# Kernel tuning notes

Measured on AMD Instinct MI355X. Metric: run time of the kernel, lower is better.

The kernel has to match this reference:

```python
import jax, jax.numpy as jnp
import numpy as np

HEAD_SIZE = 64


def setup_inputs() -> dict:
    key = jax.random.key(0)
    ks = jax.random.split(key, 4)
    B, S, H, D = 8, 4096, 768, HEAD_SIZE
    scale = 1.0 / np.sqrt(H)
    return {
        "x": jax.random.normal(ks[0], (B, S, H), dtype=jnp.float32),
        "Wq": jax.random.normal(ks[1], (H, D), dtype=jnp.float32) * scale,
        "bq": jnp.zeros((D,), dtype=jnp.float32),
        "Wk": jax.random.normal(ks[2], (H, D), dtype=jnp.float32) * scale,
        "bk": jnp.zeros((D,), dtype=jnp.float32),
        "Wv": jax.random.normal(ks[3], (H, D), dtype=jnp.float32) * scale,
        "bv": jnp.zeros((D,), dtype=jnp.float32),
    }


def reference(x, Wq, bq, Wk, bk, Wv, bv):
    # x: [B, S, H]
    B, S, H = x.shape
    D = Wq.shape[1]
    q = x @ Wq + bq  # [B, S, D]
    k = x @ Wk + bk
    v = x @ Wv + bv
    # naive full score matrix [B, S, S]
    scores = jnp.einsum("bsd,btd->bst", q, k)
    causal = jnp.tril(jnp.ones((S, S), dtype=bool))  # lower-triangular mask
    scores = jnp.where(causal[None, :, :], scores, -jnp.inf)
    attn = jax.nn.softmax(scores / jnp.sqrt(jnp.float32(D)), axis=-1)
    # dropout is identity in eval/deterministic reference
    out = jnp.einsum("bst,btd->bsd", attn, v)  # [B, S, D]
    return out
```

## Files before the change

kernel.cpp:

```cpp
#include <hip/hip_runtime.h>

typedef unsigned short u16;
typedef __bf16 bf16_t;
typedef bf16_t bf16x8 __attribute__((ext_vector_type(8)));
typedef float f32x4 __attribute__((ext_vector_type(4)));
typedef u16 u16x8 __attribute__((ext_vector_type(8)));

#define B_ 8
#define S_ 4096
#define H_ 768
#define M_ (B_ * S_)

__device__ __forceinline__ u16 f2b(float f) {
  unsigned u = __float_as_uint(f);
  u += 0x7fffu + ((u >> 16) & 1u);
  return (u16)(u >> 16);
}

__device__ __forceinline__ void gl_lds16(const void* g, void* l) {
  __builtin_amdgcn_global_load_lds(
      (const __attribute__((address_space(1))) void*)g,
      (__attribute__((address_space(3))) void*)l, 16, 0, 0);
}

__global__ __launch_bounds__(256) void wconv_k(const float* __restrict__ Wq,
                                               const float* __restrict__ Wk,
                                               const float* __restrict__ Wv,
                                               u16* __restrict__ WbT) {
  __shared__ float wt[64 * 68];
  const int tid = threadIdx.x;
  int mat = blockIdx.x / 12;
  int k0 = (blockIdx.x % 12) * 64;
  const float* W = (mat == 0) ? Wq : ((mat == 1) ? Wk : Wv);
  int r = tid >> 2, c0 = (tid & 3) * 16;
  const float* src = W + (size_t)(k0 + r) * 64 + c0;
#pragma unroll
  for (int j = 0; j < 16; j += 4)
    *(float4*)&wt[r * 68 + c0 + j] = *(const float4*)(src + j);
  __syncthreads();
  int d = tid >> 2;
  u16* dst = WbT + (size_t)(mat * 64 + d) * 768 + k0 + c0;
  u16x8 o0, o1;
#pragma unroll
  for (int j = 0; j < 8; ++j) o0[j] = f2b(wt[(c0 + j) * 68 + d]);
#pragma unroll
  for (int j = 0; j < 8; ++j) o1[j] = f2b(wt[(c0 + 8 + j) * 68 + d]);
  *(u16x8*)dst = o0;
  *(u16x8*)(dst + 8) = o1;
}

__global__ __launch_bounds__(256) void qkv_k(const float* __restrict__ x,
                                             const u16* __restrict__ WbT,
                                             const float* __restrict__ bq,
                                             const float* __restrict__ bk,
                                             const float* __restrict__ bv,
                                             u16* __restrict__ qb,
                                             u16* __restrict__ kb,
                                             u16* __restrict__ vbT) {
  __shared__ __align__(16) u16 smem[2 * 2560 + 2 * 7680];
  const int tid = threadIdx.x;
  const int w = tid >> 6, ln = tid & 15, qd = (tid >> 4) & 3;
  const int row0 = blockIdx.x * 64;

  const f32x4 z4 = {0.f, 0.f, 0.f, 0.f};
  f32x4 acc[4][3];
#pragma unroll
  for (int rt = 0; rt < 4; ++rt)
#pragma unroll
    for (int ct = 0; ct < 3; ++ct) acc[rt][ct] = z4;

  const int xr = tid >> 2, xc = (tid & 3) * 8;
  float4 xf0, xf1;
  u16x8 wf[3];

  auto load_t = [&](int kt) {
    const float* sx = x + (size_t)(row0 + xr) * 768 + kt * 32 + xc;
    xf0 = *(const float4*)sx;
    xf1 = *(const float4*)(sx + 4);
#pragma unroll
    for (int i = 0; i < 3; ++i) {
      int c = i * 256 + tid;
      int r = c >> 2, off = (c & 3) * 8;
      wf[i] = *(const u16x8*)(WbT + (size_t)r * 768 + kt * 32 + off);
    }
  };

  load_t(0);
  for (int kt = 0; kt < 24; ++kt) {
    u16* xs = smem + (kt & 1) * 2560;
    u16* wsb = smem + 5120 + (kt & 1) * 7680;
    {
      u16x8 v;
      v[0] = f2b(xf0.x); v[1] = f2b(xf0.y); v[2] = f2b(xf0.z); v[3] = f2b(xf0.w);
      v[4] = f2b(xf1.x); v[5] = f2b(xf1.y); v[6] = f2b(xf1.z); v[7] = f2b(xf1.w);
      *(u16x8*)&xs[xr * 40 + xc] = v;
#pragma unroll
      for (int i = 0; i < 3; ++i) {
        int c = i * 256 + tid;
        int r = c >> 2, off = (c & 3) * 8;
        *(u16x8*)&wsb[r * 40 + off] = wf[i];
      }
    }
    if (kt < 23) load_t(kt + 1);
    __syncthreads();
    bf16x8 af[4], bfr[3];
#pragma unroll
    for (int rt = 0; rt < 4; ++rt)
      af[rt] = *(const bf16x8*)&xs[(rt * 16 + ln) * 40 + qd * 8];
#pragma unroll
    for (int ct = 0; ct < 3; ++ct)
      bfr[ct] = *(const bf16x8*)&wsb[(w * 48 + ct * 16 + ln) * 40 + qd * 8];
#pragma unroll
    for (int rt = 0; rt < 4; ++rt)
#pragma unroll
      for (int ct = 0; ct < 3; ++ct)
        acc[rt][ct] = __builtin_amdgcn_mfma_f32_16x16x32_bf16(
            af[rt], bfr[ct], acc[rt][ct], 0, 0, 0);
    __syncthreads();
  }

  u16* vt = smem;
#pragma unroll
  for (int ct = 0; ct < 3; ++ct) {
    int col = w * 48 + ct * 16 + ln;
    int mat = col >> 6, d = col & 63;
    if (mat < 2) {
      const float* bp = (mat == 0) ? bq : bk;
      u16* op = (mat == 0) ? qb : kb;
      float bias = bp[d];
      float scale = (mat == 0) ? 0.18033688011112042f : 1.0f;
#pragma unroll
      for (int rt = 0; rt < 4; ++rt)
#pragma unroll
        for (int r = 0; r < 4; ++r)
          op[(size_t)(row0 + rt * 16 + qd * 4 + r) * 64 + d] =
              f2b((acc[rt][ct][r] + bias) * scale);
    } else {
      float bias = bv[d];
#pragma unroll
      for (int rt = 0; rt < 4; ++rt)
#pragma unroll
        for (int r = 0; r < 4; ++r)
          vt[d * 72 + rt * 16 + qd * 4 + r] = f2b(acc[rt][ct][r] + bias);
    }
  }
  __syncthreads();
  {
    int d = tid >> 2, so = (tid & 3) * 16;
    int b = row0 >> 12, s0 = row0 & 4095;
    u16* dst = vbT + ((size_t)b * 64 + d) * 4096 + s0 + so;
    *(u16x8*)dst = *(const u16x8*)&vt[d * 72 + so];
    *(u16x8*)(dst + 8) = *(const u16x8*)&vt[d * 72 + so + 8];
  }
}

__global__ __launch_bounds__(256) void attn_k(const u16* __restrict__ qb,
                                              const u16* __restrict__ kb,
                                              const u16* __restrict__ vbT,
                                              float* __restrict__ po0,
                                              float* __restrict__ po1,
                                              float* __restrict__ pl0,
                                              float* __restrict__ pl1) {
  __shared__ __align__(16) u16 ks[2][4096];
  __shared__ __align__(16) u16 vs[2][4096];
  __shared__ __align__(16) u16 ps[4 * 16 * 88];
  const int tid = threadIdx.x;
  const int w = tid >> 6, ln = tid & 15, qd = (tid >> 4) & 3;
  const int id = blockIdx.x;
  int b, qi, tstart, tcount;
  if (id < 256) {
    b = id & 7; qi = 32 + (id >> 3); tstart = 0; tcount = 32;
  } else if (id < 512) {
    b = id & 7; qi = 63 - ((id - 256) >> 3); tstart = 32; tcount = qi - 31;
  } else {
    b = id & 7; qi = 31 - ((id - 512) >> 3); tstart = 0; tcount = qi + 1;
  }
  const int q0 = qi * 64, q0w = q0 + w * 16;
  const int base = b * S_;
  const u16* kg = kb + (size_t)base * 64;
  const u16* vg = vbT + (size_t)b * 64 * 4096;

  bf16x8 qf[2];
  {
    const u16* qrow = qb + (size_t)(base + q0w + ln) * 64;
    qf[0] = *(const bf16x8*)(qrow + qd * 8);
    qf[1] = *(const bf16x8*)(qrow + 32 + qd * 8);
  }
  const f32x4 z4 = {0.f, 0.f, 0.f, 0.f};
  f32x4 o[4] = {z4, z4, z4, z4};
  float lp[4] = {0.f, 0.f, 0.f, 0.f};
  u16* psw = ps + w * (16 * 88);
  const int lr = (tid & 63) >> 3, csl = tid & 7;

  auto prefetch = [&](int bufi, int tile) {
    const u16* kt_ = kg + (size_t)tile * 4096;
    const u16* vt_ = vg + tile * 64;
#pragma unroll
    for (int i = 0; i < 2; ++i) {
      int r0 = w * 16 + i * 8;
      int r = r0 + lr;
      int c = csl ^ (r & 7);
      gl_lds16(kt_ + r * 64 + c * 8, &ks[bufi][r0 * 64]);
      gl_lds16(vt_ + (size_t)r * 4096 + c * 8, &vs[bufi][r0 * 64]);
    }
  };

  prefetch(0, tstart);
  int buf = 0;
  for (int it = 0; it < tcount; ++it) {
    __syncthreads();
    if (it + 1 < tcount) prefetch(buf ^ 1, tstart + it + 1);
    const int t0a = (tstart + it) * 64;

    f32x4 s[4] = {z4, z4, z4, z4};
#pragma unroll
    for (int kc = 0; kc < 2; ++kc) {
      int cs = (kc * 4 + qd) ^ (ln & 7);
#pragma unroll
      for (int nt = 0; nt < 4; ++nt) {
        bf16x8 bfr = *(const bf16x8*)&ks[buf][(nt * 16 + ln) * 64 + cs * 8];
        s[nt] = __builtin_amdgcn_mfma_f32_16x16x32_bf16(qf[kc], bfr, s[nt], 0, 0, 0);
      }
    }
    if (t0a == q0) {
#pragma unroll
      for (int nt = 0; nt < 4; ++nt) {
        int tg = t0a + nt * 16 + ln;
#pragma unroll
        for (int r = 0; r < 4; ++r)
          if (tg > q0w + qd * 4 + r) s[nt][r] = -INFINITY;
      }
    }
#pragma unroll
    for (int nt = 0; nt < 4; ++nt)
#pragma unroll
      for (int r = 0; r < 4; ++r) {
        float p = __builtin_amdgcn_exp2f(s[nt][r]);
        lp[r] += p;
        psw[(qd * 4 + r) * 88 + nt * 16 + ln] = f2b(p);
      }
#pragma unroll
    for (int kc = 0; kc < 2; ++kc) {
      bf16x8 afr = *(const bf16x8*)&psw[ln * 88 + kc * 32 + qd * 8];
      int cs = (kc * 4 + qd) ^ (ln & 7);
#pragma unroll
      for (int nt = 0; nt < 4; ++nt) {
        bf16x8 bfr = *(const bf16x8*)&vs[buf][(nt * 16 + ln) * 64 + cs * 8];
        o[nt] = __builtin_amdgcn_mfma_f32_16x16x32_bf16(afr, bfr, o[nt], 0, 0, 0);
      }
    }
    buf ^= 1;
  }

#pragma unroll
  for (int r = 0; r < 4; ++r) {
    float v = lp[r];
    v += __shfl_xor(v, 1); v += __shfl_xor(v, 2);
    v += __shfl_xor(v, 4); v += __shfl_xor(v, 8);
    lp[r] = v;
  }
  float* op = (tstart == 0) ? po0 : po1;
  float* lpt = (tstart == 0) ? pl0 : pl1;
#pragma unroll
  for (int r = 0; r < 4; ++r) {
    int row = base + q0w + qd * 4 + r;
#pragma unroll
    for (int nt = 0; nt < 4; ++nt)
      op[(size_t)row * 64 + nt * 16 + ln] = o[nt][r];
    if (ln == 0) lpt[row] = lp[r];
  }
}

__global__ __launch_bounds__(256) void comb_k(const float* __restrict__ po0,
                                              const float* __restrict__ po1,
                                              const float* __restrict__ pl0,
                                              const float* __restrict__ pl1,
                                              float* __restrict__ out) {
  int idx = blockIdx.x * 256 + threadIdx.x;
  int r = idx >> 4, d0 = (idx & 15) * 4;
  int qi = (r & 4095) >> 6;
  float4 a = *(const float4*)(po0 + (size_t)r * 64 + d0);
  float l = pl0[r];
  if (qi >= 32) {
    float4 c = *(const float4*)(po1 + (size_t)r * 64 + d0);
    a.x += c.x; a.y += c.y; a.z += c.z; a.w += c.w;
    l += pl1[r];
  }
  float inv = 1.0f / l;
  a.x *= inv; a.y *= inv; a.z *= inv; a.w *= inv;
  *(float4*)(out + (size_t)r * 64 + d0) = a;
}

extern "C" void kernel_launch(void* const* d_in, const int* in_sizes, int n_in,
                              void* d_out, int out_size, void* d_ws, size_t ws_size,
                              hipStream_t stream) {
  const float* x  = (const float*)d_in[0];
  const float* Wq = (const float*)d_in[1];
  const float* bq = (const float*)d_in[2];
  const float* Wk = (const float*)d_in[3];
  const float* bk = (const float*)d_in[4];
  const float* Wv = (const float*)d_in[5];
  const float* bv = (const float*)d_in[6];
  float* out = (float*)d_out;

  char* wsp = (char*)d_ws;
  u16* WbT = (u16*)wsp;
  u16* qb  = (u16*)(wsp + 294912);
  u16* kb  = (u16*)(wsp + 4489216);
  u16* vbT = (u16*)(wsp + 8683520);
  float* po0 = (float*)(wsp + 12877824);
  float* po1 = (float*)(wsp + 21266432);
  float* pl0 = (float*)(wsp + 29655040);
  float* pl1 = (float*)(wsp + 29786112);

  hipLaunchKernelGGL(wconv_k, dim3(36), dim3(256), 0, stream, Wq, Wk, Wv, WbT);
  hipLaunchKernelGGL(qkv_k, dim3(512), dim3(256), 0, stream,
                     x, WbT, bq, bk, bv, qb, kb, vbT);
  hipLaunchKernelGGL(attn_k, dim3(768), dim3(256), 0, stream,
                     qb, kb, vbT, po0, po1, pl0, pl1);
  hipLaunchKernelGGL(comb_k, dim3(2048), dim3(256), 0, stream,
                     po0, po1, pl0, pl1, out);
}
```

Measured before the change: 226.3 us.

## Use 128-row query tiles with two row-tiles per wave and split KV in halves

Each wave now handles 32 query rows (two 16-row MFMA tiles) so every K/V fragment read from LDS feeds two MFMAs, which halves LDS traffic per unit of compute. The causal work split changes to 512 blocks: each 128-row query tile is cut into two equal KV-range chunks, and the combine kernel always sums both partials. Waves skip KV tiles that lie entirely above their diagonal. In exchange, register pressure rises and there are fewer blocks, which may reduce occupancy. The diagonal tiles also need masking on more iterations.

```diff
diff --git a/kernel.cpp b/kernel.cpp
--- a/kernel.cpp
+++ b/kernel.cpp
@@ -163,33 +163,37 @@
                                               float* __restrict__ pl1) {
   __shared__ __align__(16) u16 ks[2][4096];
   __shared__ __align__(16) u16 vs[2][4096];
-  __shared__ __align__(16) u16 ps[4 * 16 * 88];
+  __shared__ __align__(16) u16 ps[4 * 32 * 72];
   const int tid = threadIdx.x;
   const int w = tid >> 6, ln = tid & 15, qd = (tid >> 4) & 3;
   const int id = blockIdx.x;
-  int b, qi, tstart, tcount;
-  if (id < 256) {
-    b = id & 7; qi = 32 + (id >> 3); tstart = 0; tcount = 32;
-  } else if (id < 512) {
-    b = id & 7; qi = 63 - ((id - 256) >> 3); tstart = 32; tcount = qi - 31;
-  } else {
-    b = id & 7; qi = 31 - ((id - 512) >> 3); tstart = 0; tcount = qi + 1;
-  }
-  const int q0 = qi * 64, q0w = q0 + w * 16;
+  const int b = id & 7;
+  const int j = id >> 3;
+  const int qi = 31 - (j >> 1);
+  const int chunk = j & 1;
+  const int tstart = chunk ? (qi + 1) : 0;
+  const int tcount = qi + 1;
+  const int q0 = qi * 128;
+  const int q0w = q0 + w * 32;
   const int base = b * S_;
   const u16* kg = kb + (size_t)base * 64;
   const u16* vg = vbT + (size_t)b * 64 * 4096;
 
-  bf16x8 qf[2];
-  {
-    const u16* qrow = qb + (size_t)(base + q0w + ln) * 64;
-    qf[0] = *(const bf16x8*)(qrow + qd * 8);
-    qf[1] = *(const bf16x8*)(qrow + 32 + qd * 8);
+  bf16x8 qf[2][2];
+#pragma unroll
+  for (int rt = 0; rt < 2; ++rt) {
+    const u16* qrow = qb + (size_t)(base + q0w + rt * 16 + ln) * 64;
+    qf[rt][0] = *(const bf16x8*)(qrow + qd * 8);
+    qf[rt][1] = *(const bf16x8*)(qrow + 32 + qd * 8);
   }
   const f32x4 z4 = {0.f, 0.f, 0.f, 0.f};
-  f32x4 o[4] = {z4, z4, z4, z4};
-  float lp[4] = {0.f, 0.f, 0.f, 0.f};
-  u16* psw = ps + w * (16 * 88);
+  f32x4 o[2][4];
+#pragma unroll
+  for (int rt = 0; rt < 2; ++rt)
+#pragma unroll
+    for (int nt = 0; nt < 4; ++nt) o[rt][nt] = z4;
+  float lp[2][4] = {{0.f, 0.f, 0.f, 0.f}, {0.f, 0.f, 0.f, 0.f}};
+  u16* psw = ps + w * (32 * 72);
   const int lr = (tid & 63) >> 3, csl = tid & 7;
 
   auto prefetch = [&](int bufi, int tile) {
@@ -212,63 +216,78 @@
     if (it + 1 < tcount) prefetch(buf ^ 1, tstart + it + 1);
     const int t0a = (tstart + it) * 64;
 
-    f32x4 s[4] = {z4, z4, z4, z4};
-#pragma unroll
-    for (int kc = 0; kc < 2; ++kc) {
-      int cs = (kc * 4 + qd) ^ (ln & 7);
-#pragma unroll
-      for (int nt = 0; nt < 4; ++nt) {
-        bf16x8 bfr = *(const bf16x8*)&ks[buf][(nt * 16 + ln) * 64 + cs * 8];
-        s[nt] = __builtin_amdgcn_mfma_f32_16x16x32_bf16(qf[kc], bfr, s[nt], 0, 0, 0);
+    if (t0a <= q0w + 31) {
+      f32x4 s0[4] = {z4, z4, z4, z4};
+      f32x4 s1[4] = {z4, z4, z4, z4};
+#pragma unroll
+      for (int kc = 0; kc < 2; ++kc) {
+        int cs = (kc * 4 + qd) ^ (ln & 7);
+#pragma unroll
+        for (int nt = 0; nt < 4; ++nt) {
+          bf16x8 bfr = *(const bf16x8*)&ks[buf][(nt * 16 + ln) * 64 + cs * 8];
+          s0[nt] = __builtin_amdgcn_mfma_f32_16x16x32_bf16(qf[0][kc], bfr, s0[nt], 0, 0, 0);
+          s1[nt] = __builtin_amdgcn_mfma_f32_16x16x32_bf16(qf[1][kc], bfr, s1[nt], 0, 0, 0);
+        }
       }
-    }
-    if (t0a == q0) {
-#pragma unroll
-      for (int nt = 0; nt < 4; ++nt) {
-        int tg = t0a + nt * 16 + ln;
-#pragma unroll
-        for (int r = 0; r < 4; ++r)
-          if (tg > q0w + qd * 4 + r) s[nt][r] = -INFINITY;
+      if (t0a + 63 > q0w) {
+#pragma unroll
+        for (int nt = 0; nt < 4; ++nt) {
+          int tg = t0a + nt * 16 + ln;
+#pragma unroll
+          for (int r = 0; r < 4; ++r) {
+            if (tg > q0w + qd * 4 + r) s0[nt][r] = -INFINITY;
+            if (tg > q0w + 16 + qd * 4 + r) s1[nt][r] = -INFINITY;
+          }
+        }
       }
-    }
-#pragma unroll
-    for (int nt = 0; nt < 4; ++nt)
-#pragma unroll
-      for (int r = 0; r < 4; ++r) {
-        float p = __builtin_amdgcn_exp2f(s[nt][r]);
-        lp[r] += p;
-        psw[(qd * 4 + r) * 88 + nt * 16 + ln] = f2b(p);
+#pragma unroll
+      for (int nt = 0; nt < 4; ++nt)
+#pragma unroll
+        for (int r = 0; r < 4; ++r) {
+          float p0 = __builtin_amdgcn_exp2f(s0[nt][r]);
+          float p1 = __builtin_amdgcn_exp2f(s1[nt][r]);
+          lp[0][r] += p0;
+          lp[1][r] += p1;
+          psw[(qd * 4 + r) * 72 + nt * 16 + ln] = f2b(p0);
+          psw[(16 + qd * 4 + r) * 72 + nt * 16 + ln] = f2b(p1);
+        }
+#pragma unroll
+      for (int kc = 0; kc < 2; ++kc) {
+        bf16x8 a0 = *(const bf16x8*)&psw[ln * 72 + kc * 32 + qd * 8];
+        bf16x8 a1 = *(const bf16x8*)&psw[(16 + ln) * 72 + kc * 32 + qd * 8];
+        int cs = (kc * 4 + qd) ^ (ln & 7);
+#pragma unroll
+        for (int nt = 0; nt < 4; ++nt) {
+          bf16x8 vfr = *(const bf16x8*)&vs[buf][(nt * 16 + ln) * 64 + cs * 8];
+          o[0][nt] = __builtin_amdgcn_mfma_f32_16x16x32_bf16(a0, vfr, o[0][nt], 0, 0, 0);
+          o[1][nt] = __builtin_amdgcn_mfma_f32_16x16x32_bf16(a1, vfr, o[1][nt], 0, 0, 0);
+        }
       }
-#pragma unroll
-    for (int kc = 0; kc < 2; ++kc) {
-      bf16x8 afr = *(const bf16x8*)&psw[ln * 88 + kc * 32 + qd * 8];
-      int cs = (kc * 4 + qd) ^ (ln & 7);
-#pragma unroll
-      for (int nt = 0; nt < 4; ++nt) {
-        bf16x8 bfr = *(const bf16x8*)&vs[buf][(nt * 16 + ln) * 64 + cs * 8];
-        o[nt] = __builtin_amdgcn_mfma_f32_16x16x32_bf16(afr, bfr, o[nt], 0, 0, 0);
-      }
     }
     buf ^= 1;
   }
 
 #pragma unroll
-  for (int r = 0; r < 4; ++r) {
-    float v = lp[r];
-    v += __shfl_xor(v, 1); v += __shfl_xor(v, 2);
-    v += __shfl_xor(v, 4); v += __shfl_xor(v, 8);
-    lp[r] = v;
-  }
+  for (int rt = 0; rt < 2; ++rt)
+#pragma unroll
+    for (int r = 0; r < 4; ++r) {
+      float v = lp[rt][r];
+      v += __shfl_xor(v, 1); v += __shfl_xor(v, 2);
+      v += __shfl_xor(v, 4); v += __shfl_xor(v, 8);
+      lp[rt][r] = v;
+    }
   float* op = (tstart == 0) ? po0 : po1;
   float* lpt = (tstart == 0) ? pl0 : pl1;
 #pragma unroll
-  for (int r = 0; r < 4; ++r) {
-    int row = base + q0w + qd * 4 + r;
-#pragma unroll
-    for (int nt = 0; nt < 4; ++nt)
-      op[(size_t)row * 64 + nt * 16 + ln] = o[nt][r];
-    if (ln == 0) lpt[row] = lp[r];
-  }
+  for (int rt = 0; rt < 2; ++rt)
+#pragma unroll
+    for (int r = 0; r < 4; ++r) {
+      int row = base + q0w + rt * 16 + qd * 4 + r;
+#pragma unroll
+      for (int nt = 0; nt < 4; ++nt)
+        op[(size_t)row * 64 + nt * 16 + ln] = o[rt][nt][r];
+      if (ln == 0) lpt[row] = lp[rt][r];
+    }
 }
 
 __global__ __launch_bounds__(256) void comb_k(const float* __restrict__ po0,
@@ -278,16 +297,14 @@
                                               float* __restrict__ out) {
   int idx = blockIdx.x * 256 + threadIdx.x;
   int r = idx >> 4, d0 = (idx & 15) * 4;
-  int qi = (r & 4095) >> 6;
   float4 a = *(const float4*)(po0 + (size_t)r * 64 + d0);
-  float l = pl0[r];
-  if (qi >= 32) {
-    float4 c = *(const float4*)(po1 + (size_t)r * 64 + d0);
-    a.x += c.x; a.y += c.y; a.z += c.z; a.w += c.w;
-    l += pl1[r];
-  }
+  float4 c = *(const float4*)(po1 + (size_t)r * 64 + d0);
+  float l = pl0[r] + pl1[r];
   float inv = 1.0f / l;
-  a.x *= inv; a.y *= inv; a.z *= inv; a.w *= inv;
+  a.x = (a.x + c.x) * inv;
+  a.y = (a.y + c.y) * inv;
+  a.z = (a.z + c.z) * inv;
+  a.w = (a.w + c.w) * inv;
   *(float4*)(out + (size_t)r * 64 + d0) = a;
 }
 
@@ -316,7 +333,7 @@
   hipLaunchKernelGGL(wconv_k, dim3(36), dim3(256), 0, stream, Wq, Wk, Wv, WbT);
   hipLaunchKernelGGL(qkv_k, dim3(512), dim3(256), 0, stream,
                      x, WbT, bq, bk, bv, qb, kb, vbT);
-  hipLaunchKernelGGL(attn_k, dim3(768), dim3(256), 0, stream,
+  hipLaunchKernelGGL(attn_k, dim3(512), dim3(256), 0, stream,
                      qb, kb, vbT, po0, po1, pl0, pl1);
   hipLaunchKernelGGL(comb_k, dim3(2048), dim3(256), 0, stream,
                      po0, po1, pl0, pl1, out);
```

Result: slower. 234.1 us (+3.4%).
